# Optimization experiments

Hardware: AMD Instinct MI355X
Metric: run time of the kernel (lower is better)

## Reference

```python
import jax, jax.numpy as jnp
import numpy as np

B, S, HID = 2, 2048, 3072
H, HKV, D = 16, 8, 256
ROPE_THETA = 10000.0
NEG_INF = -1e9


def setup_inputs() -> dict:
    key = jax.random.key(0)
    ks = jax.random.split(key, 5)
    hidden_states = jax.random.normal(ks[0], (B, S, HID), jnp.float32)
    # rotary frequencies: complex freqs_cis = cos + i*sin, shape (B, S, D//2)
    inv_freq = 1.0 / (ROPE_THETA ** (np.arange(0, D, 2, dtype=np.float32) / D))
    ang = np.arange(S, dtype=np.float32)[:, None] * inv_freq[None, :]  # (S, D//2)
    cos = jnp.asarray(np.broadcast_to(np.cos(ang)[None], (B, S, D // 2)).copy())
    sin = jnp.asarray(np.broadcast_to(np.sin(ang)[None], (B, S, D // 2)).copy())
    causal = jnp.tril(jnp.ones((S, S), dtype=bool))
    mask = jnp.where(causal, 0.0, NEG_INF).astype(jnp.float32)[None, None]  # (1,1,S,S)
    wq = jax.random.normal(ks[1], (HID, H * D), jnp.float32) * 0.02
    wk = jax.random.normal(ks[2], (HID, HKV * D), jnp.float32) * 0.02
    wv = jax.random.normal(ks[3], (HID, HKV * D), jnp.float32) * 0.02
    wo = jax.random.normal(ks[4], (H * D, HID), jnp.float32) * 0.02
    return {"hidden_states": hidden_states, "cos": cos, "sin": sin, "mask": mask,
            "wq": wq, "wk": wk, "wv": wv, "wo": wo}


def _apply_rotary(x, cos, sin):
    # x: (B, S, Hx, D). Torch code forms complex pairs (x[..., :D/2], x[..., D/2:])
    # and multiplies by freqs_cis = cos + i*sin, then re-concats real||imag halves.
    half = x.shape[-1] // 2
    x1, x2 = x[..., :half], x[..., half:]
    c = cos[:, :, None, :]  # (B, S, 1, D/2)
    s = sin[:, :, None, :]
    return jnp.concatenate([x1 * c - x2 * s, x1 * s + x2 * c], axis=-1)


def reference(hidden_states, cos, sin, mask, wq, wk, wv, wo):
    b, s, _ = hidden_states.shape
    q = (hidden_states @ wq).reshape(b, s, H, D)
    k = (hidden_states @ wk).reshape(b, s, HKV, D)
    v = (hidden_states @ wv).reshape(b, s, HKV, D)
    q = _apply_rotary(q, cos, sin)
    k = _apply_rotary(k, cos, sin)
    # GQA: group query heads per kv head instead of materializing repeated K/V
    g = H // HKV
    qg = q.reshape(b, s, HKV, g, D)
    scaling = D ** (-0.5)
    scores = jnp.einsum('bskgd,btkd->bkgst', qg, k) * scaling  # (B,HKV,G,S,S)
    scores = scores + mask[:, :, None]  # broadcast (1,1,1,S,S)
    probs = jax.nn.softmax(scores, axis=-1)
    out = jnp.einsum('bkgst,btkd->bskgd', probs, v).reshape(b, s, H * D)
    return out @ wo
```

## Files before the change

kernel.cpp:

```cpp
#include <hip/hip_runtime.h>

typedef short bf16x8 __attribute__((ext_vector_type(8)));
typedef float f32x4 __attribute__((ext_vector_type(4)));

#define S_LEN 2048
#define NHQ 16
#define NKV 8
#define HD 256

__device__ __forceinline__ unsigned short f2bf(float f){
  unsigned u = __float_as_uint(f);
  unsigned r = (u + 0x7FFFu + ((u >> 16) & 1u)) >> 16;
  return (unsigned short)r;
}
__device__ __forceinline__ float bf2f(unsigned short h){
  return __uint_as_float(((unsigned)h) << 16);
}
__device__ __forceinline__ unsigned pack2(float a, float b){
  return (unsigned)f2bf(a) | ((unsigned)f2bf(b) << 16);
}

__device__ __forceinline__ void gload_lds16(const void* g, void* l){
  __builtin_amdgcn_global_load_lds(
      (const __attribute__((address_space(1))) void*)g,
      (__attribute__((address_space(3))) void*)l, 16, 0, 0);
}

__global__ void k_conv(const float* __restrict__ in, unsigned short* __restrict__ out, int n){
  int i = (blockIdx.x * 256 + threadIdx.x) * 4;
  if (i < n){
    float4 v = *(const float4*)&in[i];
    ushort4 o;
    o.x = f2bf(v.x); o.y = f2bf(v.y); o.z = f2bf(v.z); o.w = f2bf(v.w);
    *(ushort4*)&out[i] = o;
  }
}

__global__ void k_tconv(const float* __restrict__ in, unsigned short* __restrict__ out, int R, int C){
  __shared__ float tile[32][33];
  int c0 = blockIdx.x * 32, r0 = blockIdx.y * 32;
  int tx = threadIdx.x, ty = threadIdx.y;
  for (int i = 0; i < 4; i++)
    tile[ty + i*8][tx] = in[(size_t)(r0 + ty + i*8) * C + c0 + tx];
  __syncthreads();
  for (int i = 0; i < 4; i++)
    out[(size_t)(c0 + ty + i*8) * R + r0 + tx] = f2bf(tile[tx][ty + i*8]);
}

__global__ void k_vtrans(const unsigned short* __restrict__ V, unsigned short* __restrict__ VT){
  __shared__ unsigned short tile[32][40];
  int s0 = blockIdx.x * 32, d0 = blockIdx.y * 32, bz = blockIdx.z;
  int b = bz >> 3, kv = bz & 7;
  int tx = threadIdx.x, ty = threadIdx.y;
  for (int i = 0; i < 4; i++)
    tile[ty + i*8][tx] = V[(size_t)(b * S_LEN + s0 + ty + i*8) * (NKV*HD) + kv*HD + d0 + tx];
  __syncthreads();
  for (int i = 0; i < 4; i++)
    VT[((size_t)(bz * HD + d0 + ty + i*8)) * S_LEN + s0 + tx] = tile[tx][ty + i*8];
}

__global__ void k_rope(unsigned short* buf, const float* __restrict__ cosb,
                       const float* __restrict__ sinb, int lgnh){
  int idx = blockIdx.x * 256 + threadIdx.x;
  int d = idx & 127;
  int h = (idx >> 7) & ((1 << lgnh) - 1);
  int t = idx >> (7 + lgnh);
  float c = cosb[t * 128 + d], s = sinb[t * 128 + d];
  size_t base = ((size_t)t << (lgnh + 8)) + ((size_t)h << 8) + d;
  float x1 = bf2f(buf[base]), x2 = bf2f(buf[base + 128]);
  buf[base]       = f2bf(x1 * c - x2 * s);
  buf[base + 128] = f2bf(x1 * s + x2 * c);
}

__global__ __launch_bounds__(256) void k_gemm_bt(const unsigned short* __restrict__ A,
    const unsigned short* __restrict__ Bt, void* __restrict__ Cp,
    int M, int N, int K, int out_bf16){
  __shared__ __align__(16) unsigned short smem[2 * 128 * 64];
  unsigned short* As = smem;
  unsigned short* Bs = smem + 128 * 64;
  int tid = threadIdx.x;
  int lane = tid & 63, wave = tid >> 6, quad = lane >> 4, l16 = lane & 15;
  int wm = wave >> 1, wn = wave & 1;
  int nx = gridDim.x;
  int flat = blockIdx.y * nx + blockIdx.x;
  int cpx = (nx * gridDim.y) >> 3;
  int swz = (flat & 7) * cpx + (flat >> 3);
  int bm0 = (swz / nx) * 128, bn0 = (swz % nx) * 128;
  const unsigned short* Ag = &A[(size_t)bm0 * K];
  const unsigned short* Bg = &Bt[(size_t)bn0 * K];
  int srow = lane >> 3;
  int spc  = lane & 7;
  f32x4 acc[4][4] = {};
  for (int k0 = 0; k0 < K; k0 += 64){
    __syncthreads();
    for (int it = 0; it < 4; it++){
      int win = it * 4 + wave;
      int row = win * 8 + srow;
      int c   = spc ^ (row & 7);
      gload_lds16(&Ag[(size_t)row * K + k0 + c * 8], &As[win * 512]);
      gload_lds16(&Bg[(size_t)row * K + k0 + c * 8], &Bs[win * 512]);
    }
    __syncthreads();
    for (int ks = 0; ks < 2; ks++){
      bf16x8 af[4], bfr[4];
      for (int mt = 0; mt < 4; mt++){
        int row = wm * 64 + mt * 16 + l16;
        int pc = (ks * 4 + quad) ^ (row & 7);
        af[mt] = *(const bf16x8*)&As[row * 64 + pc * 8];
      }
      for (int nt = 0; nt < 4; nt++){
        int row = wn * 64 + nt * 16 + l16;
        int pc = (ks * 4 + quad) ^ (row & 7);
        bfr[nt] = *(const bf16x8*)&Bs[row * 64 + pc * 8];
      }
      for (int mt = 0; mt < 4; mt++)
        for (int nt = 0; nt < 4; nt++)
          acc[mt][nt] = __builtin_amdgcn_mfma_f32_16x16x32_bf16(af[mt], bfr[nt], acc[mt][nt], 0, 0, 0);
    }
  }
  float* Ct = (float*)smem;
  for (int p = 0; p < 2; p++){
    __syncthreads();
    if (wm == p){
      for (int mt = 0; mt < 4; mt++)
        for (int nt = 0; nt < 4; nt++)
          for (int r = 0; r < 4; r++)
            Ct[(mt * 16 + quad * 4 + r) * 128 + wn * 64 + nt * 16 + l16] = acc[mt][nt][r];
    }
    __syncthreads();
    if (out_bf16){
      unsigned short* O = (unsigned short*)Cp;
      for (int j = 0; j < 4; j++){
        int chunk = j * 256 + tid;
        int row = chunk >> 4, col = (chunk & 15) * 8;
        const float* src = &Ct[row * 128 + col];
        uint4 o;
        o.x = pack2(src[0], src[1]);
        o.y = pack2(src[2], src[3]);
        o.z = pack2(src[4], src[5]);
        o.w = pack2(src[6], src[7]);
        *(uint4*)&O[(size_t)(bm0 + p * 64 + row) * N + bn0 + col] = o;
      }
    } else {
      float* O = (float*)Cp;
      for (int j = 0; j < 8; j++){
        int chunk = j * 256 + tid;
        int row = chunk >> 5, col = (chunk & 31) * 4;
        *(float4*)&O[(size_t)(bm0 + p * 64 + row) * N + bn0 + col] = *(const float4*)&Ct[row * 128 + col];
      }
    }
  }
}

__global__ __launch_bounds__(512, 2) void k_flash(const unsigned short* __restrict__ Q,
    const unsigned short* __restrict__ Kg, const unsigned short* __restrict__ VTg,
    unsigned short* __restrict__ Og){
  __shared__ __align__(16) unsigned short smem[2 * (32*264 + 256*40) + 8 * 16 * 40];
  const int BUFSZ = 32*264 + 256*40;
  int tid = threadIdx.x;
  int lane = tid & 63, wave = tid >> 6, quad = lane >> 4, l16 = lane & 15;
  int hig = wave & 1, rowgrp = wave >> 1;
  int bkv = blockIdx.x, p = blockIdx.y;
  int b = bkv >> 3, kv = bkv & 7;
  int h = kv * 2 + hig;
  const float L2E = 1.4426950408889634f;
  const float scale = 0.0625f;

  size_t kgbase = (size_t)(b * S_LEN) * (NKV*HD) + (size_t)kv * HD;
  size_t vtbase = ((size_t)(b * NKV + kv) * HD) * S_LEN;
  unsigned short* Ps = smem + 2 * BUFSZ + wave * (16 * 40);

  for (int ph = 0; ph < 2; ph++){
    int qt = ph ? (31 - p) : p;
    int qmin = qt * 64 + rowgrp * 16;
    int nkt = qt * 2 + 2;

    bf16x8 qf[8];
    {
      size_t qoff = ((size_t)(b * S_LEN + qt * 64 + rowgrp * 16 + l16)) * (NHQ * HD) + (size_t)h * HD;
      for (int ks = 0; ks < 8; ks++)
        qf[ks] = *(const bf16x8*)&Q[qoff + ks * 32 + quad * 8];
    }
    f32x4 acc[16] = {};
    float mrow[4], lrow[4];
    for (int r = 0; r < 4; r++){ mrow[r] = -1e30f; lrow[r] = 0.f; }

    uint4 stk[2], stv[2];
    for (int it = 0; it < 2; it++){
      int slot = it * 512 + tid;
      int kr = slot >> 5, c = slot & 31;
      stk[it] = *(const uint4*)&Kg[kgbase + (size_t)(kr) * (NKV*HD) + c * 8];
      int dd = slot >> 2, c2 = slot & 3;
      stv[it] = *(const uint4*)&VTg[vtbase + (size_t)dd * S_LEN + c2 * 8];
    }

    for (int kt = 0; kt < nkt; kt++){
      unsigned short* Ks  = smem + (kt & 1) * BUFSZ;
      unsigned short* VTs = Ks + 32 * 264;
      for (int it = 0; it < 2; it++){
        int slot = it * 512 + tid;
        int kr = slot >> 5, c = slot & 31;
        *(uint4*)&Ks[kr * 264 + c * 8] = stk[it];
        int dd = slot >> 2, c2 = slot & 3;
        *(uint4*)&VTs[dd * 40 + c2 * 8] = stv[it];
      }
      if (kt + 1 < nkt){
        for (int it = 0; it < 2; it++){
          int slot = it * 512 + tid;
          int kr = slot >> 5, c = slot & 31;
          stk[it] = *(const uint4*)&Kg[kgbase + (size_t)((kt + 1) * 32 + kr) * (NKV*HD) + c * 8];
          int dd = slot >> 2, c2 = slot & 3;
          stv[it] = *(const uint4*)&VTg[vtbase + (size_t)dd * S_LEN + (kt + 1) * 32 + c2 * 8];
        }
      }
      __syncthreads();
      if (kt * 32 > qmin + 15) continue;

      f32x4 sv[2] = {};
      __builtin_amdgcn_s_setprio(1);
      for (int ks = 0; ks < 8; ks++){
        for (int nt = 0; nt < 2; nt++){
          bf16x8 kf = *(const bf16x8*)&Ks[(nt * 16 + l16) * 264 + ks * 32 + quad * 8];
          sv[nt] = __builtin_amdgcn_mfma_f32_16x16x32_bf16(qf[ks], kf, sv[nt], 0, 0, 0);
        }
      }
      __builtin_amdgcn_s_setprio(0);
      float pv[2][4], tmax[4];
      for (int r = 0; r < 4; r++){
        int qr = qmin + quad * 4 + r;
        float mx = -1e30f;
        for (int nt = 0; nt < 2; nt++){
          int key = kt * 32 + nt * 16 + l16;
          float v = sv[nt][r] * scale;
          if (key > qr) v = -1e30f;
          pv[nt][r] = v;
          mx = fmaxf(mx, v);
        }
        tmax[r] = mx;
      }
      for (int off = 1; off < 16; off <<= 1)
        for (int r = 0; r < 4; r++)
          tmax[r] = fmaxf(tmax[r], __shfl_xor(tmax[r], off, 64));
      int grow = (tmax[0] > mrow[0]) | (tmax[1] > mrow[1]) |
                 (tmax[2] > mrow[2]) | (tmax[3] > mrow[3]);
      if (grow){
        float alpha[4];
        for (int r = 0; r < 4; r++){
          float mn = fmaxf(mrow[r], tmax[r]);
          alpha[r] = exp2f((mrow[r] - mn) * L2E);
          mrow[r] = mn;
          lrow[r] *= alpha[r];
        }
        for (int i = 0; i < 16; i++)
          for (int r = 0; r < 4; r++) acc[i][r] *= alpha[r];
      }
      float pb[2][4], psum[4] = {0.f, 0.f, 0.f, 0.f};
      for (int nt = 0; nt < 2; nt++)
        for (int r = 0; r < 4; r++){
          float pe = exp2f((pv[nt][r] - mrow[r]) * L2E);
          pb[nt][r] = pe; psum[r] += pe;
        }
      for (int off = 1; off < 16; off <<= 1)
        for (int r = 0; r < 4; r++)
          psum[r] += __shfl_xor(psum[r], off, 64);
      for (int r = 0; r < 4; r++) lrow[r] += psum[r];
      for (int nt = 0; nt < 2; nt++)
        for (int r = 0; r < 4; r++)
          Ps[(quad * 4 + r) * 40 + nt * 16 + l16] = f2bf(pb[nt][r]);
      bf16x8 pa = *(const bf16x8*)&Ps[l16 * 40 + quad * 8];
      __builtin_amdgcn_s_setprio(1);
      for (int nt = 0; nt < 16; nt++){
        bf16x8 vf = *(const bf16x8*)&VTs[(nt * 16 + l16) * 40 + quad * 8];
        acc[nt] = __builtin_amdgcn_mfma_f32_16x16x32_bf16(pa, vf, acc[nt], 0, 0, 0);
      }
      __builtin_amdgcn_s_setprio(0);
    }
    float inv[4];
    for (int r = 0; r < 4; r++) inv[r] = 1.0f / lrow[r];
    __syncthreads();
    unsigned short* Ot = smem + wave * (16 * 256);
    for (int nt = 0; nt < 16; nt++)
      for (int r = 0; r < 4; r++)
        Ot[(quad * 4 + r) * 256 + nt * 16 + l16] = f2bf(acc[nt][r] * inv[r]);
    size_t obase = ((size_t)(b * S_LEN + qt * 64 + rowgrp * 16)) * (NHQ * HD) + (size_t)h * HD;
    for (int j = 0; j < 8; j++){
      int chunk = j * 64 + lane;
      int row = chunk >> 5, col = (chunk & 31) * 8;
      *(uint4*)&Og[obase + (size_t)row * (NHQ * HD) + col] = *(const uint4*)&Ot[row * 256 + col];
    }
    __syncthreads();
  }
}

extern "C" void kernel_launch(void* const* d_in, const int* in_sizes, int n_in,
                              void* d_out, int out_size, void* d_ws, size_t ws_size,
                              hipStream_t stream){
  const float* hid  = (const float*)d_in[0];
  const float* cosb = (const float*)d_in[1];
  const float* sinb = (const float*)d_in[2];
  const float* wq = (const float*)d_in[4];
  const float* wk = (const float*)d_in[5];
  const float* wv = (const float*)d_in[6];
  const float* wo = (const float*)d_in[7];

  char* ws = (char*)d_ws;
  size_t off = 0;
  auto alloc = [&](size_t bytes) -> void* {
    void* p = ws + off; off += (bytes + 255) & ~(size_t)255; return p;
  };
  unsigned short* Xbf = (unsigned short*)alloc(4096ull * 3072 * 2);
  unsigned short* WqT = (unsigned short*)alloc(4096ull * 3072 * 2);
  unsigned short* WkT = (unsigned short*)alloc(2048ull * 3072 * 2);
  unsigned short* WvT = (unsigned short*)alloc(2048ull * 3072 * 2);
  unsigned short* WoT = (unsigned short*)alloc(3072ull * 4096 * 2);
  unsigned short* Qb  = (unsigned short*)alloc(4096ull * 4096 * 2);
  unsigned short* Kb  = (unsigned short*)alloc(4096ull * 2048 * 2);
  unsigned short* Vb  = (unsigned short*)alloc(4096ull * 2048 * 2);
  unsigned short* VTb = (unsigned short*)alloc(4096ull * 2048 * 2);
  unsigned short* Ab  = (unsigned short*)alloc(4096ull * 4096 * 2);

  k_conv<<<12288, 256, 0, stream>>>(hid, Xbf, 4096 * 3072);
  k_tconv<<<dim3(128, 96), dim3(32, 8), 0, stream>>>(wq, WqT, 3072, 4096);
  k_tconv<<<dim3(64, 96),  dim3(32, 8), 0, stream>>>(wk, WkT, 3072, 2048);
  k_tconv<<<dim3(64, 96),  dim3(32, 8), 0, stream>>>(wv, WvT, 3072, 2048);
  k_tconv<<<dim3(96, 128), dim3(32, 8), 0, stream>>>(wo, WoT, 4096, 3072);
  k_gemm_bt<<<dim3(32, 32), 256, 0, stream>>>(Xbf, WqT, Qb, 4096, 4096, 3072, 1);
  k_gemm_bt<<<dim3(16, 32), 256, 0, stream>>>(Xbf, WkT, Kb, 4096, 2048, 3072, 1);
  k_gemm_bt<<<dim3(16, 32), 256, 0, stream>>>(Xbf, WvT, Vb, 4096, 2048, 3072, 1);
  k_rope<<<32768, 256, 0, stream>>>(Qb, cosb, sinb, 4);
  k_rope<<<16384, 256, 0, stream>>>(Kb, cosb, sinb, 3);
  k_vtrans<<<dim3(64, 8, 16), dim3(32, 8), 0, stream>>>(Vb, VTb);
  k_flash<<<dim3(16, 16), 512, 0, stream>>>(Qb, Kb, VTb, Ab);
  k_gemm_bt<<<dim3(24, 32), 256, 0, stream>>>(Ab, WoT, d_out, 4096, 3072, 4096, 0);
}
```

Measured before the change: 906.5 us.

## Split flash attention per query head, swizzle K in LDS, vectorize RoPE

The flash kernel now runs one query head per block: 256 threads and a third grid dimension, where before a 512-thread block covered both heads of a GQA pair. The grid grows to 512 blocks. The double-buffered K/V LDS is replaced by a single buffer with an XOR-swizzled K layout to avoid bank conflicts, plus an extra barrier per tile. Each K/V tile is now loaded twice, once per head, so K/V global traffic doubles, though much of it may hit in L2. RoPE is vectorized to 8 elements per thread with 16-byte loads and stores, cutting thread count and memory transactions.

```diff
diff --git a/kernel.cpp b/kernel.cpp
--- a/kernel.cpp
+++ b/kernel.cpp
@@ -62,14 +62,26 @@
 __global__ void k_rope(unsigned short* buf, const float* __restrict__ cosb,
                        const float* __restrict__ sinb, int lgnh){
   int idx = blockIdx.x * 256 + threadIdx.x;
-  int d = idx & 127;
-  int h = (idx >> 7) & ((1 << lgnh) - 1);
-  int t = idx >> (7 + lgnh);
-  float c = cosb[t * 128 + d], s = sinb[t * 128 + d];
-  size_t base = ((size_t)t << (lgnh + 8)) + ((size_t)h << 8) + d;
-  float x1 = bf2f(buf[base]), x2 = bf2f(buf[base + 128]);
-  buf[base]       = f2bf(x1 * c - x2 * s);
-  buf[base + 128] = f2bf(x1 * s + x2 * c);
+  int d0 = (idx & 15) * 8;
+  int h = (idx >> 4) & ((1 << lgnh) - 1);
+  int t = idx >> (4 + lgnh);
+  float ca[8], sa[8];
+  *(float4*)&ca[0] = *(const float4*)&cosb[t * 128 + d0];
+  *(float4*)&ca[4] = *(const float4*)&cosb[t * 128 + d0 + 4];
+  *(float4*)&sa[0] = *(const float4*)&sinb[t * 128 + d0];
+  *(float4*)&sa[4] = *(const float4*)&sinb[t * 128 + d0 + 4];
+  size_t base = ((size_t)t << (lgnh + 8)) + ((size_t)h << 8) + d0;
+  bf16x8 x1 = *(const bf16x8*)&buf[base];
+  bf16x8 x2 = *(const bf16x8*)&buf[base + 128];
+  bf16x8 o1, o2;
+  #pragma unroll
+  for (int j = 0; j < 8; j++){
+    float f1 = bf2f((unsigned short)x1[j]), f2 = bf2f((unsigned short)x2[j]);
+    o1[j] = (short)f2bf(f1 * ca[j] - f2 * sa[j]);
+    o2[j] = (short)f2bf(f1 * sa[j] + f2 * ca[j]);
+  }
+  *(bf16x8*)&buf[base] = o1;
+  *(bf16x8*)&buf[base + 128] = o2;
 }
 
 __global__ __launch_bounds__(256) void k_gemm_bt(const unsigned short* __restrict__ A,
@@ -152,15 +164,15 @@
   }
 }
 
-__global__ __launch_bounds__(512, 2) void k_flash(const unsigned short* __restrict__ Q,
+__global__ __launch_bounds__(256, 2) void k_flash(const unsigned short* __restrict__ Q,
     const unsigned short* __restrict__ Kg, const unsigned short* __restrict__ VTg,
     unsigned short* __restrict__ Og){
-  __shared__ __align__(16) unsigned short smem[2 * (32*264 + 256*40) + 8 * 16 * 40];
-  const int BUFSZ = 32*264 + 256*40;
+  __shared__ __align__(16) unsigned short smem[32*256 + 256*36 + 4*16*40];
+  unsigned short* Ks  = smem;
+  unsigned short* VTs = smem + 32 * 256;
   int tid = threadIdx.x;
   int lane = tid & 63, wave = tid >> 6, quad = lane >> 4, l16 = lane & 15;
-  int hig = wave & 1, rowgrp = wave >> 1;
-  int bkv = blockIdx.x, p = blockIdx.y;
+  int bkv = blockIdx.x, p = blockIdx.y, hig = blockIdx.z;
   int b = bkv >> 3, kv = bkv & 7;
   int h = kv * 2 + hig;
   const float L2E = 1.4426950408889634f;
@@ -168,16 +180,16 @@
 
   size_t kgbase = (size_t)(b * S_LEN) * (NKV*HD) + (size_t)kv * HD;
   size_t vtbase = ((size_t)(b * NKV + kv) * HD) * S_LEN;
-  unsigned short* Ps = smem + 2 * BUFSZ + wave * (16 * 40);
+  unsigned short* Ps = smem + 32*256 + 256*36 + wave * (16 * 40);
 
   for (int ph = 0; ph < 2; ph++){
     int qt = ph ? (31 - p) : p;
-    int qmin = qt * 64 + rowgrp * 16;
+    int qmin = qt * 64 + wave * 16;
     int nkt = qt * 2 + 2;
 
     bf16x8 qf[8];
     {
-      size_t qoff = ((size_t)(b * S_LEN + qt * 64 + rowgrp * 16 + l16)) * (NHQ * HD) + (size_t)h * HD;
+      size_t qoff = ((size_t)(b * S_LEN + qt * 64 + wave * 16 + l16)) * (NHQ * HD) + (size_t)h * HD;
       for (int ks = 0; ks < 8; ks++)
         qf[ks] = *(const bf16x8*)&Q[qoff + ks * 32 + quad * 8];
     }
@@ -185,104 +197,114 @@
     float mrow[4], lrow[4];
     for (int r = 0; r < 4; r++){ mrow[r] = -1e30f; lrow[r] = 0.f; }
 
-    uint4 stk[2], stv[2];
-    for (int it = 0; it < 2; it++){
-      int slot = it * 512 + tid;
+    uint4 stk[4], stv[4];
+    for (int it = 0; it < 4; it++){
+      int slot = it * 256 + tid;
       int kr = slot >> 5, c = slot & 31;
-      stk[it] = *(const uint4*)&Kg[kgbase + (size_t)(kr) * (NKV*HD) + c * 8];
+      stk[it] = *(const uint4*)&Kg[kgbase + (size_t)kr * (NKV*HD) + c * 8];
       int dd = slot >> 2, c2 = slot & 3;
       stv[it] = *(const uint4*)&VTg[vtbase + (size_t)dd * S_LEN + c2 * 8];
     }
+    for (int it = 0; it < 4; it++){
+      int slot = it * 256 + tid;
+      int kr = slot >> 5, c = slot & 31;
+      *(uint4*)&Ks[kr * 256 + (c ^ kr) * 8] = stk[it];
+      int dd = slot >> 2, c2 = slot & 3;
+      *(uint4*)&VTs[dd * 36 + c2 * 8] = stv[it];
+    }
+    __syncthreads();
 
     for (int kt = 0; kt < nkt; kt++){
-      unsigned short* Ks  = smem + (kt & 1) * BUFSZ;
-      unsigned short* VTs = Ks + 32 * 264;
-      for (int it = 0; it < 2; it++){
-        int slot = it * 512 + tid;
-        int kr = slot >> 5, c = slot & 31;
-        *(uint4*)&Ks[kr * 264 + c * 8] = stk[it];
-        int dd = slot >> 2, c2 = slot & 3;
-        *(uint4*)&VTs[dd * 40 + c2 * 8] = stv[it];
-      }
-      if (kt + 1 < nkt){
-        for (int it = 0; it < 2; it++){
-          int slot = it * 512 + tid;
+      int have_next = (kt + 1 < nkt);
+      if (have_next){
+        for (int it = 0; it < 4; it++){
+          int slot = it * 256 + tid;
           int kr = slot >> 5, c = slot & 31;
           stk[it] = *(const uint4*)&Kg[kgbase + (size_t)((kt + 1) * 32 + kr) * (NKV*HD) + c * 8];
           int dd = slot >> 2, c2 = slot & 3;
           stv[it] = *(const uint4*)&VTg[vtbase + (size_t)dd * S_LEN + (kt + 1) * 32 + c2 * 8];
         }
       }
+      if (kt * 32 <= qmin + 15){
+        f32x4 sv[2] = {};
+        __builtin_amdgcn_s_setprio(1);
+        for (int ks = 0; ks < 8; ks++){
+          for (int nt = 0; nt < 2; nt++){
+            int row = nt * 16 + l16;
+            bf16x8 kf = *(const bf16x8*)&Ks[row * 256 + ((ks * 4 + quad) ^ row) * 8];
+            sv[nt] = __builtin_amdgcn_mfma_f32_16x16x32_bf16(qf[ks], kf, sv[nt], 0, 0, 0);
+          }
+        }
+        __builtin_amdgcn_s_setprio(0);
+        float pv[2][4], tmax[4];
+        for (int r = 0; r < 4; r++){
+          int qr = qmin + quad * 4 + r;
+          float mx = -1e30f;
+          for (int nt = 0; nt < 2; nt++){
+            int key = kt * 32 + nt * 16 + l16;
+            float v = sv[nt][r] * scale;
+            if (key > qr) v = -1e30f;
+            pv[nt][r] = v;
+            mx = fmaxf(mx, v);
+          }
+          tmax[r] = mx;
+        }
+        for (int off = 1; off < 16; off <<= 1)
+          for (int r = 0; r < 4; r++)
+            tmax[r] = fmaxf(tmax[r], __shfl_xor(tmax[r], off, 64));
+        int grow = (tmax[0] > mrow[0]) | (tmax[1] > mrow[1]) |
+                   (tmax[2] > mrow[2]) | (tmax[3] > mrow[3]);
+        if (grow){
+          float alpha[4];
+          for (int r = 0; r < 4; r++){
+            float mn = fmaxf(mrow[r], tmax[r]);
+            alpha[r] = exp2f((mrow[r] - mn) * L2E);
+            mrow[r] = mn;
+            lrow[r] *= alpha[r];
+          }
+          for (int i = 0; i < 16; i++)
+            for (int r = 0; r < 4; r++) acc[i][r] *= alpha[r];
+        }
+        float pb[2][4], psum[4] = {0.f, 0.f, 0.f, 0.f};
+        for (int nt = 0; nt < 2; nt++)
+          for (int r = 0; r < 4; r++){
+            float pe = exp2f((pv[nt][r] - mrow[r]) * L2E);
+            pb[nt][r] = pe; psum[r] += pe;
+          }
+        for (int off = 1; off < 16; off <<= 1)
+          for (int r = 0; r < 4; r++)
+            psum[r] += __shfl_xor(psum[r], off, 64);
+        for (int r = 0; r < 4; r++) lrow[r] += psum[r];
+        for (int nt = 0; nt < 2; nt++)
+          for (int r = 0; r < 4; r++)
+            Ps[(quad * 4 + r) * 40 + nt * 16 + l16] = f2bf(pb[nt][r]);
+        bf16x8 pa = *(const bf16x8*)&Ps[l16 * 40 + quad * 8];
+        __builtin_amdgcn_s_setprio(1);
+        for (int nt = 0; nt < 16; nt++){
+          bf16x8 vf = *(const bf16x8*)&VTs[(nt * 16 + l16) * 36 + quad * 8];
+          acc[nt] = __builtin_amdgcn_mfma_f32_16x16x32_bf16(pa, vf, acc[nt], 0, 0, 0);
+        }
+        __builtin_amdgcn_s_setprio(0);
+      }
       __syncthreads();
-      if (kt * 32 > qmin + 15) continue;
-
-      f32x4 sv[2] = {};
-      __builtin_amdgcn_s_setprio(1);
-      for (int ks = 0; ks < 8; ks++){
-        for (int nt = 0; nt < 2; nt++){
-          bf16x8 kf = *(const bf16x8*)&Ks[(nt * 16 + l16) * 264 + ks * 32 + quad * 8];
-          sv[nt] = __builtin_amdgcn_mfma_f32_16x16x32_bf16(qf[ks], kf, sv[nt], 0, 0, 0);
-        }
-      }
-      __builtin_amdgcn_s_setprio(0);
-      float pv[2][4], tmax[4];
-      for (int r = 0; r < 4; r++){
-        int qr = qmin + quad * 4 + r;
-        float mx = -1e30f;
-        for (int nt = 0; nt < 2; nt++){
-          int key = kt * 32 + nt * 16 + l16;
-          float v = sv[nt][r] * scale;
-          if (key > qr) v = -1e30f;
-          pv[nt][r] = v;
-          mx = fmaxf(mx, v);
-        }
-        tmax[r] = mx;
-      }
-      for (int off = 1; off < 16; off <<= 1)
-        for (int r = 0; r < 4; r++)
-          tmax[r] = fmaxf(tmax[r], __shfl_xor(tmax[r], off, 64));
-      int grow = (tmax[0] > mrow[0]) | (tmax[1] > mrow[1]) |
-                 (tmax[2] > mrow[2]) | (tmax[3] > mrow[3]);
-      if (grow){
-        float alpha[4];
-        for (int r = 0; r < 4; r++){
-          float mn = fmaxf(mrow[r], tmax[r]);
-          alpha[r] = exp2f((mrow[r] - mn) * L2E);
-          mrow[r] = mn;
-          lrow[r] *= alpha[r];
-        }
-        for (int i = 0; i < 16; i++)
-          for (int r = 0; r < 4; r++) acc[i][r] *= alpha[r];
-      }
-      float pb[2][4], psum[4] = {0.f, 0.f, 0.f, 0.f};
-      for (int nt = 0; nt < 2; nt++)
-        for (int r = 0; r < 4; r++){
-          float pe = exp2f((pv[nt][r] - mrow[r]) * L2E);
-          pb[nt][r] = pe; psum[r] += pe;
-        }
-      for (int off = 1; off < 16; off <<= 1)
-        for (int r = 0; r < 4; r++)
-          psum[r] += __shfl_xor(psum[r], off, 64);
-      for (int r = 0; r < 4; r++) lrow[r] += psum[r];
-      for (int nt = 0; nt < 2; nt++)
-        for (int r = 0; r < 4; r++)
-          Ps[(quad * 4 + r) * 40 + nt * 16 + l16] = f2bf(pb[nt][r]);
-      bf16x8 pa = *(const bf16x8*)&Ps[l16 * 40 + quad * 8];
-      __builtin_amdgcn_s_setprio(1);
-      for (int nt = 0; nt < 16; nt++){
-        bf16x8 vf = *(const bf16x8*)&VTs[(nt * 16 + l16) * 40 + quad * 8];
-        acc[nt] = __builtin_amdgcn_mfma_f32_16x16x32_bf16(pa, vf, acc[nt], 0, 0, 0);
-      }
-      __builtin_amdgcn_s_setprio(0);
+      if (have_next){
+        for (int it = 0; it < 4; it++){
+          int slot = it * 256 + tid;
+          int kr = slot >> 5, c = slot & 31;
+          *(uint4*)&Ks[kr * 256 + (c ^ kr) * 8] = stk[it];
+          int dd = slot >> 2, c2 = slot & 3;
+          *(uint4*)&VTs[dd * 36 + c2 * 8] = stv[it];
+        }
+      }
+      __syncthreads();
     }
     float inv[4];
     for (int r = 0; r < 4; r++) inv[r] = 1.0f / lrow[r];
-    __syncthreads();
     unsigned short* Ot = smem + wave * (16 * 256);
     for (int nt = 0; nt < 16; nt++)
       for (int r = 0; r < 4; r++)
         Ot[(quad * 4 + r) * 256 + nt * 16 + l16] = f2bf(acc[nt][r] * inv[r]);
-    size_t obase = ((size_t)(b * S_LEN + qt * 64 + rowgrp * 16)) * (NHQ * HD) + (size_t)h * HD;
+    size_t obase = ((size_t)(b * S_LEN + qt * 64 + wave * 16)) * (NHQ * HD) + (size_t)h * HD;
     for (int j = 0; j < 8; j++){
       int chunk = j * 64 + lane;
       int row = chunk >> 5, col = (chunk & 31) * 8;
@@ -327,9 +349,9 @@
   k_gemm_bt<<<dim3(32, 32), 256, 0, stream>>>(Xbf, WqT, Qb, 4096, 4096, 3072, 1);
   k_gemm_bt<<<dim3(16, 32), 256, 0, stream>>>(Xbf, WkT, Kb, 4096, 2048, 3072, 1);
   k_gemm_bt<<<dim3(16, 32), 256, 0, stream>>>(Xbf, WvT, Vb, 4096, 2048, 3072, 1);
-  k_rope<<<32768, 256, 0, stream>>>(Qb, cosb, sinb, 4);
-  k_rope<<<16384, 256, 0, stream>>>(Kb, cosb, sinb, 3);
+  k_rope<<<4096, 256, 0, stream>>>(Qb, cosb, sinb, 4);
+  k_rope<<<2048, 256, 0, stream>>>(Kb, cosb, sinb, 3);
   k_vtrans<<<dim3(64, 8, 16), dim3(32, 8), 0, stream>>>(Vb, VTb);
-  k_flash<<<dim3(16, 16), 512, 0, stream>>>(Qb, Kb, VTb, Ab);
+  k_flash<<<dim3(16, 16, 2), 256, 0, stream>>>(Qb, Kb, VTb, Ab);
   k_gemm_bt<<<dim3(24, 32), 256, 0, stream>>>(Ab, WoT, d_out, 4096, 3072, 4096, 0);
 }
```

Result: slower. 1.183 ms (+30.5%).
